# Optimization experiments

Hardware: AMD Instinct MI355X
Metric: run time of the kernel (lower is better)

Reference implementation:

```python
import jax, jax.numpy as jnp
import numpy as np


def mha(x, mask, wq, bq, wk, bk, wv, bv, wo, bo, n_heads):
    # Flaubert/XLM MultiHeadAttention (eval mode, dropout = identity).
    bs, qlen, dim = x.shape
    dph = dim // n_heads

    def split_heads(t):  # (bs, qlen, dim) -> (bs, n_heads, qlen, dph)
        return t.reshape(bs, qlen, n_heads, dph).transpose(0, 2, 1, 3)

    q = split_heads(x @ wq + bq) / jnp.sqrt(jnp.asarray(dph, x.dtype))
    k = split_heads(x @ wk + bk)
    v = split_heads(x @ wv + bv)

    scores = jnp.einsum('bhqd,bhkd->bhqk', q, k)  # (bs, h, qlen, klen)
    neg = jnp.finfo(scores.dtype).min
    scores = jnp.where((mask == 0)[:, None, None, :], neg, scores)
    weights = jax.nn.softmax(scores, axis=-1)
    ctx = jnp.einsum('bhqk,bhkd->bhqd', weights, v)
    ctx = ctx.transpose(0, 2, 1, 3).reshape(bs, qlen, dim)
    return ctx @ wo + bo


def setup_inputs() -> dict:
    key = jax.random.key(0)
    ks = jax.random.split(key, 20)
    bs, slen = 4, 1024
    d0, d1 = 192, 66
    std = 0.02
    inp = {
        'x': jax.random.normal(ks[0], (bs, slen, d0), jnp.float32),
        'y': jax.random.normal(ks[1], (bs, slen, d1), jnp.float32),
        'mask0': jax.random.randint(ks[2], (bs, slen), 0, 2, jnp.int32),
        'mask1': jax.random.randint(ks[3], (bs, slen), 0, 2, jnp.int32),
    }
    names0 = ['q0', 'k0', 'v0', 'o0']
    names1 = ['q1', 'k1', 'v1', 'o1']
    for i, n in enumerate(names0):
        inp[n + '_w'] = jax.random.normal(ks[4 + i], (d0, d0), jnp.float32) * std
        inp[n + '_b'] = jnp.zeros((d0,), jnp.float32)
    for i, n in enumerate(names1):
        inp[n + '_w'] = jax.random.normal(ks[8 + i], (d1, d1), jnp.float32) * std
        inp[n + '_b'] = jnp.zeros((d1,), jnp.float32)
    return inp


def reference(x, y, mask0, mask1,
              q0_w, q0_b, k0_w, k0_b, v0_w, v0_b, o0_w, o0_b,
              q1_w, q1_b, k1_w, k1_b, v1_w, v1_b, o1_w, o1_b):
    out0 = mha(x, mask0, q0_w, q0_b, k0_w, k0_b, v0_w, v0_b, o0_w, o0_b, n_heads=16)
    out1 = mha(y, mask1, q1_w, q1_b, k1_w, k1_b, v1_w, v1_b, o1_w, o1_b, n_heads=11)
    return (out0, out1)
```

## Files before the change

### kernel.cpp

```cpp
#include <hip/hip_runtime.h>
#include <math.h>


#define BS 4
#define SLEN 1024

#define Q0_OFF 0
#define C0_OFF 786432
#define Q1_OFF 1572864
#define C1_OFF 1843200
#define K0H_OFF 2113536
#define V0T_OFF 2506752
#define K1H_OFF 2899968
#define V1T_OFF 3080192

#define OUT0_SIZE 786432

typedef _Float16 f16x2 __attribute__((ext_vector_type(2)));
typedef _Float16 f16x4 __attribute__((ext_vector_type(4)));
typedef _Float16 f16x8 __attribute__((ext_vector_type(8)));
typedef float f32x4 __attribute__((ext_vector_type(4)));

union F16x8U { f16x8 v8; f16x4 v4[2]; };

__device__ __forceinline__ void mfma_chunk(const _Float16* sA, const _Float16* sWT,
                                           int wv, int lane, f32x4 acc[4])
{
  const int col = lane & 15, grp = lane >> 4;
#pragma unroll
  for (int ks = 0; ks < 2; ++ks) {
    const f16x8 bf = *(const f16x8*)(sWT + (wv * 16 + col) * 72 + ks * 32 + grp * 8);
#pragma unroll
    for (int mt = 0; mt < 4; ++mt) {
      const f16x8 af = *(const f16x8*)(sA + (mt * 16 + col) * 72 + ks * 32 + grp * 8);
      acc[mt] = __builtin_amdgcn_mfma_f32_16x16x32_f16(af, bf, acc[mt], 0, 0, 0);
    }
  }
}

__device__ __forceinline__ void mfma_chunk_split(
    const _Float16* sAh, const _Float16* sAl,
    const _Float16* sWTh, const _Float16* sWTl,
    int wv, int lane, f32x4 acc[4])
{
  const int col = lane & 15, grp = lane >> 4;
#pragma unroll
  for (int ks = 0; ks < 2; ++ks) {
    const int boff = (wv * 16 + col) * 72 + ks * 32 + grp * 8;
    const f16x8 bh = *(const f16x8*)(sWTh + boff);
    const f16x8 bl = *(const f16x8*)(sWTl + boff);
#pragma unroll
    for (int mt = 0; mt < 4; ++mt) {
      const int aoff = (mt * 16 + col) * 72 + ks * 32 + grp * 8;
      const f16x8 ah = *(const f16x8*)(sAh + aoff);
      const f16x8 al = *(const f16x8*)(sAl + aoff);
      acc[mt] = __builtin_amdgcn_mfma_f32_16x16x32_f16(ah, bh, acc[mt], 0, 0, 0);
      acc[mt] = __builtin_amdgcn_mfma_f32_16x16x32_f16(ah, bl, acc[mt], 0, 0, 0);
      acc[mt] = __builtin_amdgcn_mfma_f32_16x16x32_f16(al, bh, acc[mt], 0, 0, 0);
    }
  }
}

template <int DIM>
__device__ __forceinline__ void stage_chunk(const float* __restrict__ A, int row0,
                                            int kc, const float* __restrict__ W,
                                            int col0, _Float16* sA, _Float16* sWT,
                                            int tid)
{
  for (int idx = tid; idx < 2048; idx += 256) {
    const int m = idx >> 5, k = (idx & 31) * 2;
    float2 v = make_float2(0.f, 0.f);
    if (kc + k < DIM) v = *(const float2*)(A + (size_t)(row0 + m) * DIM + kc + k);
    *(f16x2*)(sA + m * 72 + k) = (f16x2){(_Float16)v.x, (_Float16)v.y};
  }
  for (int idx = tid; idx < 2048; idx += 256) {
    const int k = idx >> 5, n = (idx & 31) * 2;
    float2 v = make_float2(0.f, 0.f);
    if (kc + k < DIM && col0 + n < DIM)
      v = *(const float2*)(W + (size_t)(kc + k) * DIM + col0 + n);
    sWT[n * 72 + k] = (_Float16)v.x;
    sWT[(n + 1) * 72 + k] = (_Float16)v.y;
  }
}

template <int DIM>
__device__ __forceinline__ void stage_chunk_split(
    const float* __restrict__ A, int row0, int kc,
    const float* __restrict__ W, int col0,
    _Float16* sAh, _Float16* sAl, _Float16* sWTh, _Float16* sWTl, int tid)
{
  for (int idx = tid; idx < 2048; idx += 256) {
    const int m = idx >> 5, k = (idx & 31) * 2;
    float2 v = make_float2(0.f, 0.f);
    if (kc + k < DIM) v = *(const float2*)(A + (size_t)(row0 + m) * DIM + kc + k);
    const _Float16 hx = (_Float16)v.x, hy = (_Float16)v.y;
    *(f16x2*)(sAh + m * 72 + k) = (f16x2){hx, hy};
    *(f16x2*)(sAl + m * 72 + k) =
        (f16x2){(_Float16)(v.x - (float)hx), (_Float16)(v.y - (float)hy)};
  }
  for (int idx = tid; idx < 2048; idx += 256) {
    const int k = idx >> 5, n = (idx & 31) * 2;
    float2 v = make_float2(0.f, 0.f);
    if (kc + k < DIM && col0 + n < DIM)
      v = *(const float2*)(W + (size_t)(kc + k) * DIM + col0 + n);
    const _Float16 hx = (_Float16)v.x, hy = (_Float16)v.y;
    sWTh[n * 72 + k] = hx;
    sWTh[(n + 1) * 72 + k] = hy;
    sWTl[n * 72 + k] = (_Float16)(v.x - (float)hx);
    sWTl[(n + 1) * 72 + k] = (_Float16)(v.y - (float)hy);
  }
}

template <int DIM, int H, int DPH, int NT, int NCH, int KST>
__device__ void qkv_impl(int bid, const float* __restrict__ X,
                         const float* __restrict__ qw, const float* __restrict__ qb,
                         const float* __restrict__ kw, const float* __restrict__ kb,
                         const float* __restrict__ vw, const float* __restrict__ vb,
                         float* __restrict__ qo, _Float16* __restrict__ kh,
                         _Float16* __restrict__ vth, char* smem)
{
  const int mt64 = bid & 63;
  const int rest = bid >> 6;
  const int mat = rest / NT;
  const int nt = rest % NT;
  const int row0 = mt64 * 64, col0 = nt * 64;

  const float* W = (mat == 0) ? qw : (mat == 1) ? kw : vw;
  const float* B = (mat == 0) ? qb : (mat == 1) ? kb : vb;
  const float scale = (mat == 0) ? (1.0f / sqrtf((float)DPH)) : 1.0f;

  _Float16* sA = (_Float16*)smem;
  _Float16* sWT = sA + 64 * 72;

  const int tid = threadIdx.x;
  const int wv = tid >> 6, lane = tid & 63;
  f32x4 acc[4] = {{0.f,0.f,0.f,0.f},{0.f,0.f,0.f,0.f},{0.f,0.f,0.f,0.f},{0.f,0.f,0.f,0.f}};

  for (int c = 0; c < NCH; ++c) {
    __syncthreads();
    stage_chunk<DIM>(X, row0, c * 64, W, col0, sA, sWT, tid);
    __syncthreads();
    mfma_chunk(sA, sWT, wv, lane, acc);
  }

  const int col = lane & 15, grp = lane >> 4;
  const int cidx = col0 + wv * 16 + col;
  if (cidx < DIM) {
    const float bias = B[cidx];
    const int h = cidx / DPH, d = cidx % DPH;
#pragma unroll
    for (int mt = 0; mt < 4; ++mt) {
#pragma unroll
      for (int r = 0; r < 4; ++r) {
        const int m = row0 + mt * 16 + grp * 4 + r;
        const int b = m >> 10, s = m & 1023;
        const float v = acc[mt][r] + bias;
        const int bh = b * H + h;
        if (mat == 0)
          qo[(size_t)((bh << 10) + s) * DPH + d] = v * scale;
        else if (mat == 1)
          kh[(size_t)((bh << 10) + s) * KST + d] = (_Float16)v;
        else
          vth[((size_t)(bh * DPH + d) << 10) + s] = (_Float16)v;
      }
    }
  }
}

__global__ __launch_bounds__(256) void qkv_kernel(
    const float* __restrict__ x, const float* __restrict__ y,
    const float* __restrict__ q0w, const float* __restrict__ q0b,
    const float* __restrict__ k0w, const float* __restrict__ k0b,
    const float* __restrict__ v0w, const float* __restrict__ v0b,
    const float* __restrict__ q1w, const float* __restrict__ q1b,
    const float* __restrict__ k1w, const float* __restrict__ k1b,
    const float* __restrict__ v1w, const float* __restrict__ v1b,
    float* __restrict__ ws)
{
  extern __shared__ char smem[];
  _Float16* hws = (_Float16*)ws;
  const int bid = blockIdx.x;
  if (bid < 576)
    qkv_impl<192, 16, 12, 3, 3, 12>(bid, x, q0w, q0b, k0w, k0b, v0w, v0b,
                                    ws + Q0_OFF, hws + 2 * (size_t)K0H_OFF,
                                    hws + 2 * (size_t)V0T_OFF, smem);
  else
    qkv_impl<66, 11, 6, 2, 2, 8>(bid - 576, y, q1w, q1b, k1w, k1b, v1w, v1b,
                                 ws + Q1_OFF, hws + 2 * (size_t)K1H_OFF,
                                 hws + 2 * (size_t)V1T_OFF, smem);
}

template <int H, int DPH, int SKP>
__device__ void attn_impl(int bid, const float* __restrict__ qg,
                          const _Float16* __restrict__ kh,
                          const _Float16* __restrict__ vth,
                          const int* __restrict__ mask,
                          float* __restrict__ ctx, char* smem)
{
  constexpr int CH = 128;
  constexpr int NCH = SLEN / CH;
  constexpr int KBUF = CH * SKP + 32;
  constexpr int VST = 136;
  constexpr int VROWS = DPH + 1;
  constexpr int PST = 44;
  constexpr int PWAVE = 16 * PST;

  _Float16* sK = (_Float16*)smem;
  _Float16* sVT = sK + 2 * KBUF;
  float* sB = (float*)(sVT + 2 * VROWS * VST);
  _Float16* sP = (_Float16*)(sB + 2 * CH);

  const int bh = bid >> 4;
  const int b = bh / H;
  const int h = bh % H;
  const int tid = threadIdx.x;

  const float* qb_ = qg + (size_t)bh * SLEN * DPH;
  const _Float16* kb_ = kh + (size_t)bh * SLEN * SKP;
  const _Float16* vb_ = vth + ((size_t)bh * DPH << 10);
  const int* mb_ = mask + b * SLEN;

  if (tid < 64) sK[(tid >> 5) * KBUF + CH * SKP + (tid & 31)] = (_Float16)0.f;
  for (int idx = tid; idx < 2 * CH; idx += 256) {
    const int pb = idx / CH, q = idx % CH;
    sVT[(pb * VROWS + DPH) * VST + q] = (_Float16)1.f;
  }

  const int wave = tid >> 6, lane = tid & 63;
  const int col = lane & 15, grp = lane >> 4;
  const int qtile = (bid & 15) * 4 + wave;

  f16x8 aq;
  {
    const int qrow = qtile * 16 + col;
#pragma unroll
    for (int j = 0; j < 8; ++j) {
      const int d = grp * 8 + j;
      aq[j] = (d < DPH) ? (_Float16)qb_[(size_t)qrow * DPH + d] : (_Float16)0.f;
    }
  }

  auto stage = [&](int cc, int pb) {
    const uint4* srcK = (const uint4*)(kb_ + (size_t)cc * CH * SKP);
    uint4* dstK = (uint4*)(sK + pb * KBUF);
    for (int idx = tid; idx < CH * SKP / 8; idx += 256) dstK[idx] = srcK[idx];
    _Float16* dV = sVT + pb * VROWS * VST;
    for (int idx = tid; idx < DPH * 16; idx += 256) {
      const int d = idx >> 4, q = idx & 15;
      *(uint4*)(dV + d * VST + q * 8) =
          ((const uint4*)(vb_ + ((size_t)d << 10) + cc * CH))[q];
    }
    float* dB = sB + pb * CH;
    for (int idx = tid; idx < CH; idx += 256)
      dB[idx] = mb_[cc * CH + idx] ? 0.f : -64.f;
  };

  stage(0, 0);
  __syncthreads();

  f32x4 Oacc[2] = {{0.f,0.f,0.f,0.f},{0.f,0.f,0.f,0.f}};
  const int de = (col <= DPH) ? col : 0;

#pragma unroll 1
  for (int c = 0; c < NCH; ++c) {
    const int p = c & 1;
    if (c + 1 < NCH) stage(c + 1, p ^ 1);

    const _Float16* sKp = sK + p * KBUF;
    const _Float16* sVp = sVT + p * VROWS * VST;
    const float* sBp = sB + p * CH;

#pragma unroll
    for (int kc = 0; kc < CH / 32; ++kc) {
      F16x8U kf0, kf1;
      {
        const _Float16* kp0 = sKp + ((kc * 2) * 16 + col) * SKP + grp * 8;
        const _Float16* kp1 = sKp + ((kc * 2 + 1) * 16 + col) * SKP + grp * 8;
        kf0.v4[0] = *(const f16x4*)kp0;
        kf0.v4[1] = *(const f16x4*)(kp0 + 4);
        kf1.v4[0] = *(const f16x4*)kp1;
        kf1.v4[1] = *(const f16x4*)(kp1 + 4);
      }
      const float bb0 = sBp[kc * 32 + col];
      const float bb1 = sBp[kc * 32 + 16 + col];
      const f32x4 S0 = __builtin_amdgcn_mfma_f32_16x16x32_f16(
          aq, kf0.v8, (f32x4){bb0, bb0, bb0, bb0}, 0, 0, 0);
      const f32x4 S1 = __builtin_amdgcn_mfma_f32_16x16x32_f16(
          aq, kf1.v8, (f32x4){bb1, bb1, bb1, bb1}, 0, 0, 0);

      _Float16* pw = sP + wave * PWAVE + col;
#pragma unroll
      for (int r = 0; r < 4; ++r) {
        pw[(grp * 4 + r) * PST] = (_Float16)__expf(S0[r]);
        pw[(grp * 4 + r) * PST + 16] = (_Float16)__expf(S1[r]);
      }

      const f16x8 vf = *(const f16x8*)(sVp + de * VST + kc * 32 + grp * 8);
      F16x8U pf;
      {
        const _Float16* pr = sP + wave * PWAVE + col * PST + grp * 8;
        pf.v4[0] = *(const f16x4*)pr;
        pf.v4[1] = *(const f16x4*)(pr + 4);
      }
      Oacc[kc & 1] =
          __builtin_amdgcn_mfma_f32_16x16x32_f16(pf.v8, vf, Oacc[kc & 1], 0, 0, 0);
    }
    __syncthreads();
  }

  f32x4 Osum;
#pragma unroll
  for (int r = 0; r < 4; ++r) Osum[r] = Oacc[0][r] + Oacc[1][r];
  float lq[4];
#pragma unroll
  for (int r = 0; r < 4; ++r) lq[r] = __shfl(Osum[r], (lane & 48) + DPH);
  if (col < DPH) {
    const int qrow0 = qtile * 16;
#pragma unroll
    for (int r = 0; r < 4; ++r) {
      const int row = qrow0 + grp * 4 + r;
      ctx[(size_t)(b * SLEN + row) * (H * DPH) + h * DPH + col] = Osum[r] / lq[r];
    }
  }
}

__global__ __launch_bounds__(256) void attn_kernel(
    const int* __restrict__ mask0, const int* __restrict__ mask1,
    float* __restrict__ ws)
{
  extern __shared__ char smem[];
  _Float16* hws = (_Float16*)ws;
  const int bid = blockIdx.x;
  if (bid < 1024)
    attn_impl<16, 12, 12>(bid, ws + Q0_OFF, hws + 2 * (size_t)K0H_OFF,
                          hws + 2 * (size_t)V0T_OFF, mask0, ws + C0_OFF, smem);
  else
    attn_impl<11, 6, 8>(bid - 1024, ws + Q1_OFF, hws + 2 * (size_t)K1H_OFF,
                        hws + 2 * (size_t)V1T_OFF, mask1, ws + C1_OFF, smem);
}

template <int DIM, int NCH>
__device__ void oproj_impl(int bid, const float* __restrict__ Cx,
                           const float* __restrict__ ow, const float* __restrict__ ob,
                           float* __restrict__ out, char* smem)
{
  const int mt64 = bid & 63;
  const int nt = bid >> 6;
  const int row0 = mt64 * 64, col0 = nt * 64;

  _Float16* sAh = (_Float16*)smem;
  _Float16* sAl = sAh + 64 * 72;
  _Float16* sWTh = sAl + 64 * 72;
  _Float16* sWTl = sWTh + 64 * 72;

  const int tid = threadIdx.x;
  const int wv = tid >> 6, lane = tid & 63;
  f32x4 acc[4] = {{0.f,0.f,0.f,0.f},{0.f,0.f,0.f,0.f},{0.f,0.f,0.f,0.f},{0.f,0.f,0.f,0.f}};

  for (int c = 0; c < NCH; ++c) {
    __syncthreads();
    stage_chunk_split<DIM>(Cx, row0, c * 64, ow, col0, sAh, sAl, sWTh, sWTl, tid);
    __syncthreads();
    mfma_chunk_split(sAh, sAl, sWTh, sWTl, wv, lane, acc);
  }

  const int col = lane & 15, grp = lane >> 4;
  const int cidx = col0 + wv * 16 + col;
  if (cidx < DIM) {
    const float bias = ob[cidx];
#pragma unroll
    for (int mt = 0; mt < 4; ++mt) {
#pragma unroll
      for (int r = 0; r < 4; ++r) {
        const int m = row0 + mt * 16 + grp * 4 + r;
        out[(size_t)m * DIM + cidx] = acc[mt][r] + bias;
      }
    }
  }
}

__global__ __launch_bounds__(256) void oproj_kernel(
    const float* __restrict__ o0w, const float* __restrict__ o0b,
    const float* __restrict__ o1w, const float* __restrict__ o1b,
    float* __restrict__ ws, float* __restrict__ out)
{
  extern __shared__ char smem[];
  const int bid = blockIdx.x;
  if (bid < 192)
    oproj_impl<192, 3>(bid, ws + C0_OFF, o0w, o0b, out, smem);
  else
    oproj_impl<66, 2>(bid - 192, ws + C1_OFF, o1w, o1b, out + OUT0_SIZE, smem);
}

extern "C" void kernel_launch(void* const* d_in, const int* in_sizes, int n_in,
                              void* d_out, int out_size, void* d_ws, size_t ws_size,
                              hipStream_t stream)
{
  const float* x = (const float*)d_in[0];
  const float* y = (const float*)d_in[1];
  const int* mask0 = (const int*)d_in[2];
  const int* mask1 = (const int*)d_in[3];
  const float* q0w = (const float*)d_in[4];  const float* q0b = (const float*)d_in[5];
  const float* k0w = (const float*)d_in[6];  const float* k0b = (const float*)d_in[7];
  const float* v0w = (const float*)d_in[8];  const float* v0b = (const float*)d_in[9];
  const float* o0w = (const float*)d_in[10]; const float* o0b = (const float*)d_in[11];
  const float* q1w = (const float*)d_in[12]; const float* q1b = (const float*)d_in[13];
  const float* k1w = (const float*)d_in[14]; const float* k1b = (const float*)d_in[15];
  const float* v1w = (const float*)d_in[16]; const float* v1b = (const float*)d_in[17];
  const float* o1w = (const float*)d_in[18]; const float* o1b = (const float*)d_in[19];

  float* ws = (float*)d_ws;
  float* out = (float*)d_out;

  const int qkv_smem = 2 * 64 * 72 * 2;
  const int oproj_smem = 4 * 64 * 72 * 2;
  const int attn_smem = 2 * (128 * 12 + 32) * 2 + 2 * 13 * 136 * 2
                      + 2 * 128 * 4 + 4 * (16 * 44) * 2;

  qkv_kernel<<<960, 256, qkv_smem, stream>>>(x, y, q0w, q0b, k0w, k0b, v0w, v0b,
                                             q1w, q1b, k1w, k1b, v1w, v1b, ws);
  attn_kernel<<<1728, 256, attn_smem, stream>>>(mask0, mask1, ws);
  oproj_kernel<<<320, 256, oproj_smem, stream>>>(o0w, o0b, o1w, o1b, ws, out);
}
```

Baseline: 168.0 us.

## Software-pipeline attention inner loop with register prefetch and exp2 softmax

The attention kernel now loads the next K/V/mask chunk into registers at the top of each iteration and writes it to shared memory only after compute, so global-load latency overlaps with the MFMA work. The QK^T MFMA for sub-chunk kc+1 is issued before the PV MFMA of sub-chunk kc, using a double-buffered per-wave P scratch so the exp and P store can overlap the matrix ops. The Q scale folds in log2(e) so the cheaper exp2 instruction replaces __expf, and the mask bias becomes -100 in the base-2 domain. This costs more registers and a larger P shared-memory region, which may lower occupancy.

```diff
diff --git a/kernel.cpp b/kernel.cpp
--- a/kernel.cpp
+++ b/kernel.cpp
@@ -15,6 +15,12 @@
 #define V1T_OFF 3080192
 
 #define OUT0_SIZE 786432
+
+#if __has_builtin(__builtin_amdgcn_exp2f)
+#define EXP2(x) __builtin_amdgcn_exp2f(x)
+#else
+#define EXP2(x) __expf((x) * 0.69314718056f)
+#endif
 
 typedef _Float16 f16x2 __attribute__((ext_vector_type(2)));
 typedef _Float16 f16x4 __attribute__((ext_vector_type(4)));
@@ -127,7 +133,7 @@
 
   const float* W = (mat == 0) ? qw : (mat == 1) ? kw : vw;
   const float* B = (mat == 0) ? qb : (mat == 1) ? kb : vb;
-  const float scale = (mat == 0) ? (1.0f / sqrtf((float)DPH)) : 1.0f;
+  const float scale = (mat == 0) ? (1.44269504089f / sqrtf((float)DPH)) : 1.0f;
 
   _Float16* sA = (_Float16*)smem;
   _Float16* sWT = sA + 64 * 72;
@@ -199,6 +205,7 @@
 {
   constexpr int CH = 128;
   constexpr int NCH = SLEN / CH;
+  constexpr int NKC = CH / 32;
   constexpr int KBUF = CH * SKP + 32;
   constexpr int VST = 136;
   constexpr int VROWS = DPH + 1;
@@ -240,22 +247,24 @@
     }
   }
 
-  auto stage = [&](int cc, int pb) {
-    const uint4* srcK = (const uint4*)(kb_ + (size_t)cc * CH * SKP);
-    uint4* dstK = (uint4*)(sK + pb * KBUF);
-    for (int idx = tid; idx < CH * SKP / 8; idx += 256) dstK[idx] = srcK[idx];
-    _Float16* dV = sVT + pb * VROWS * VST;
-    for (int idx = tid; idx < DPH * 16; idx += 256) {
-      const int d = idx >> 4, q = idx & 15;
-      *(uint4*)(dV + d * VST + q * 8) =
-          ((const uint4*)(vb_ + ((size_t)d << 10) + cc * CH))[q];
-    }
-    float* dB = sB + pb * CH;
-    for (int idx = tid; idx < CH; idx += 256)
-      dB[idx] = mb_[cc * CH + idx] ? 0.f : -64.f;
+  constexpr int kN = CH * SKP / 8;
+  constexpr int vN = DPH * 16;
+  const int vd = tid >> 4, vq = tid & 15;
+  uint4 pk, pv;
+  int pm = 0;
+  auto prefetch = [&](int cc) {
+    if (tid < kN) pk = ((const uint4*)(kb_ + (size_t)cc * CH * SKP))[tid];
+    if (tid < vN) pv = ((const uint4*)(vb_ + ((size_t)vd << 10) + cc * CH))[vq];
+    if (tid < CH) pm = mb_[cc * CH + tid];
   };
-
-  stage(0, 0);
+  auto commit = [&](int pb) {
+    if (tid < kN) ((uint4*)(sK + pb * KBUF))[tid] = pk;
+    if (tid < vN) *(uint4*)(sVT + (pb * VROWS + vd) * VST + vq * 8) = pv;
+    if (tid < CH) sB[pb * CH + tid] = pm ? 0.f : -100.f;
+  };
+
+  prefetch(0);
+  commit(0);
   __syncthreads();
 
   f32x4 Oacc[2] = {{0.f,0.f,0.f,0.f},{0.f,0.f,0.f,0.f}};
@@ -264,47 +273,76 @@
 #pragma unroll 1
   for (int c = 0; c < NCH; ++c) {
     const int p = c & 1;
-    if (c + 1 < NCH) stage(c + 1, p ^ 1);
+    if (c + 1 < NCH) prefetch(c + 1);
 
     const _Float16* sKp = sK + p * KBUF;
     const _Float16* sVp = sVT + p * VROWS * VST;
     const float* sBp = sB + p * CH;
 
-#pragma unroll
-    for (int kc = 0; kc < CH / 32; ++kc) {
+    f32x4 S0, S1;
+    {
       F16x8U kf0, kf1;
-      {
-        const _Float16* kp0 = sKp + ((kc * 2) * 16 + col) * SKP + grp * 8;
-        const _Float16* kp1 = sKp + ((kc * 2 + 1) * 16 + col) * SKP + grp * 8;
-        kf0.v4[0] = *(const f16x4*)kp0;
-        kf0.v4[1] = *(const f16x4*)(kp0 + 4);
-        kf1.v4[0] = *(const f16x4*)kp1;
-        kf1.v4[1] = *(const f16x4*)(kp1 + 4);
+      const _Float16* kp0 = sKp + col * SKP + grp * 8;
+      const _Float16* kp1 = sKp + (16 + col) * SKP + grp * 8;
+      kf0.v4[0] = *(const f16x4*)kp0; kf0.v4[1] = *(const f16x4*)(kp0 + 4);
+      kf1.v4[0] = *(const f16x4*)kp1; kf1.v4[1] = *(const f16x4*)(kp1 + 4);
+      const float bb0 = sBp[col], bb1 = sBp[16 + col];
+      S0 = __builtin_amdgcn_mfma_f32_16x16x32_f16(
+          aq, kf0.v8, (f32x4){bb0, bb0, bb0, bb0}, 0, 0, 0);
+      S1 = __builtin_amdgcn_mfma_f32_16x16x32_f16(
+          aq, kf1.v8, (f32x4){bb1, bb1, bb1, bb1}, 0, 0, 0);
+    }
+
+#pragma unroll
+    for (int kc = 0; kc < NKC; ++kc) {
+      f32x4 S0n, S1n;
+      if (kc + 1 < NKC) {
+        F16x8U kf0, kf1;
+        const _Float16* kp0 = sKp + ((kc + 1) * 32 + col) * SKP + grp * 8;
+        const _Float16* kp1 = sKp + ((kc + 1) * 32 + 16 + col) * SKP + grp * 8;
+        kf0.v4[0] = *(const f16x4*)kp0; kf0.v4[1] = *(const f16x4*)(kp0 + 4);
+        kf1.v4[0] = *(const f16x4*)kp1; kf1.v4[1] = *(const f16x4*)(kp1 + 4);
+        const float bb0 = sBp[(kc + 1) * 32 + col];
+        const float bb1 = sBp[(kc + 1) * 32 + 16 + col];
+        S0n = __builtin_amdgcn_mfma_f32_16x16x32_f16(
+            aq, kf0.v8, (f32x4){bb0, bb0, bb0, bb0}, 0, 0, 0);
+        S1n = __builtin_amdgcn_mfma_f32_16x16x32_f16(
+            aq, kf1.v8, (f32x4){bb1, bb1, bb1, bb1}, 0, 0, 0);
       }
-      const float bb0 = sBp[kc * 32 + col];
-      const float bb1 = sBp[kc * 32 + 16 + col];
-      const f32x4 S0 = __builtin_amdgcn_mfma_f32_16x16x32_f16(
-          aq, kf0.v8, (f32x4){bb0, bb0, bb0, bb0}, 0, 0, 0);
-      const f32x4 S1 = __builtin_amdgcn_mfma_f32_16x16x32_f16(
-          aq, kf1.v8, (f32x4){bb1, bb1, bb1, bb1}, 0, 0, 0);
-
-      _Float16* pw = sP + wave * PWAVE + col;
+
+      _Float16* pw = sP + (wave * 2 + (kc & 1)) * PWAVE + col;
 #pragma unroll
       for (int r = 0; r < 4; ++r) {
-        pw[(grp * 4 + r) * PST] = (_Float16)__expf(S0[r]);
-        pw[(grp * 4 + r) * PST + 16] = (_Float16)__expf(S1[r]);
+        pw[(grp * 4 + r) * PST] = (_Float16)EXP2(S0[r]);
+        pw[(grp * 4 + r) * PST + 16] = (_Float16)EXP2(S1[r]);
       }
 
-      const f16x8 vf = *(const f16x8*)(sVp + de * VST + kc * 32 + grp * 8);
-      F16x8U pf;
-      {
-        const _Float16* pr = sP + wave * PWAVE + col * PST + grp * 8;
+      if (kc > 0) {
+        const f16x8 vf = *(const f16x8*)(sVp + de * VST + (kc - 1) * 32 + grp * 8);
+        F16x8U pf;
+        const _Float16* pr =
+            sP + (wave * 2 + ((kc - 1) & 1)) * PWAVE + col * PST + grp * 8;
         pf.v4[0] = *(const f16x4*)pr;
         pf.v4[1] = *(const f16x4*)(pr + 4);
+        Oacc[(kc - 1) & 1] = __builtin_amdgcn_mfma_f32_16x16x32_f16(
+            pf.v8, vf, Oacc[(kc - 1) & 1], 0, 0, 0);
       }
-      Oacc[kc & 1] =
-          __builtin_amdgcn_mfma_f32_16x16x32_f16(pf.v8, vf, Oacc[kc & 1], 0, 0, 0);
-    }
+      S0 = S0n; S1 = S1n;
+    }
+
+    {
+      constexpr int kl = NKC - 1;
+      const f16x8 vf = *(const f16x8*)(sVp + de * VST + kl * 32 + grp * 8);
+      F16x8U pf;
+      const _Float16* pr =
+          sP + (wave * 2 + (kl & 1)) * PWAVE + col * PST + grp * 8;
+      pf.v4[0] = *(const f16x4*)pr;
+      pf.v4[1] = *(const f16x4*)(pr + 4);
+      Oacc[kl & 1] = __builtin_amdgcn_mfma_f32_16x16x32_f16(
+          pf.v8, vf, Oacc[kl & 1], 0, 0, 0);
+    }
+
+    if (c + 1 < NCH) commit(p ^ 1);
     __syncthreads();
   }
 
@@ -415,7 +453,7 @@
   const int qkv_smem = 2 * 64 * 72 * 2;
   const int oproj_smem = 4 * 64 * 72 * 2;
   const int attn_smem = 2 * (128 * 12 + 32) * 2 + 2 * 13 * 136 * 2
-                      + 2 * 128 * 4 + 4 * (16 * 44) * 2;
+                      + 2 * 128 * 4 + 4 * 2 * (16 * 44) * 2;
 
   qkv_kernel<<<960, 256, qkv_smem, stream>>>(x, y, q0w, q0b, k0w, k0b, v0w, v0b,
                                              q1w, q1b, k1w, k1b, v1w, v1b, ws);
```

After: 167.2 us. Within noise of the previous version (-0.5%).
